# Performance work log

Hardware: AMD Instinct MI355X
Metric: run time of the kernel (lower is better)

## Reference

```python
import jax, jax.numpy as jnp
import numpy as np

V, E, H = 32000, 512, 1024
B, T = 32, 64

def setup_inputs() -> dict:
    key = jax.random.key(0)
    ks = jax.random.split(key, 8)
    return {
        "x": jax.random.randint(ks[0], (B, T), 0, V, dtype=jnp.int32),
        "state_h": jax.random.normal(ks[1], (B, H), dtype=jnp.float32),
        "state_c": jax.random.normal(ks[2], (B, H), dtype=jnp.float32),
        "emb_table": jax.random.normal(ks[3], (V, E), dtype=jnp.float32) * 0.02,
        "W": jax.random.normal(ks[4], (E, 4 * H), dtype=jnp.float32) * (1.0 / np.sqrt(E)),
        "U": jax.random.normal(ks[5], (H, 4 * H), dtype=jnp.float32) * (1.0 / np.sqrt(H)),
        "b": jnp.zeros((4 * H,), dtype=jnp.float32),
        "dense_W": jax.random.normal(ks[6], (H, V), dtype=jnp.float32) * (1.0 / np.sqrt(H)),
        "dense_b": jnp.zeros((V,), dtype=jnp.float32),
    }

def _lstm(emb, h0, c0, W, U, b):
    # Precompute input projections for all timesteps: [B,T,4H]
    xW = jnp.einsum('bte,eg->btg', emb, W) + b
    def step(carry, xw_t):
        h, c = carry
        z = xw_t + h @ U  # [B,4H]
        i, f, g, o = jnp.split(z, 4, axis=-1)  # Keras gate order i,f,c,o
        i = jax.nn.sigmoid(i)
        f = jax.nn.sigmoid(f)
        g = jnp.tanh(g)
        o = jax.nn.sigmoid(o)
        c = f * c + i * g
        h = o * jnp.tanh(c)
        return (h, c), h
    (h, c), hs = jax.lax.scan(step, (h0, c0), xW.transpose(1, 0, 2))
    return hs.transpose(1, 0, 2), h, c  # [B,T,H], [B,H], [B,H]

def reference(x, state_h, state_c, emb_table, W, U, b, dense_W, dense_b):
    emb = emb_table[x]  # [B,T,E]
    seq, h, c = _lstm(emb, state_h, state_c, W, U, b)
    logits = jnp.einsum('bth,hv->btv', seq, dense_W) + dense_b  # [B,T,V]
    return logits, h, c
```

## Files before the change

### kernel.cpp

```cpp
#include <hip/hip_runtime.h>

typedef unsigned short u16;
typedef __bf16 bf16x8 __attribute__((ext_vector_type(8)));
typedef float f32x4 __attribute__((ext_vector_type(4)));
typedef u16 u16x8 __attribute__((ext_vector_type(8)));
typedef u16 u16x4 __attribute__((ext_vector_type(4)));

#define T_STEPS 64
#define BATCH 32
#define HDIM 1024
#define EDIM 512
#define VDIM 32000
#define GDIM 4096

__device__ __forceinline__ u16 f2b(float v) {
  unsigned x = __float_as_uint(v);
  return (u16)((x + 0x7fffu + ((x >> 16) & 1u)) >> 16);
}

__device__ __forceinline__ void gload16(const void* g, void* l) {
  __builtin_amdgcn_global_load_lds(
      (const __attribute__((address_space(1))) void*)g,
      (__attribute__((address_space(3))) void*)l, 16, 0, 0);
}

__device__ __forceinline__ f32x4 mfma16(bf16x8 a, bf16x8 b, f32x4 c) {
  return __builtin_amdgcn_mfma_f32_16x16x32_bf16(a, b, c, 0, 0, 0);
}


__global__ __launch_bounds__(256) void gather_emb_k(
    const int* __restrict__ x, const float* __restrict__ emb,
    u16* __restrict__ A) {
  int bt = blockIdx.x;
  int tok = x[bt];
  const float4* src = (const float4*)(emb + (size_t)tok * EDIM);
  u16x4* dst = (u16x4*)(A + (size_t)bt * EDIM);
  if (threadIdx.x < 128) {
    float4 v = src[threadIdx.x];
    u16x4 o = {f2b(v.x), f2b(v.y), f2b(v.z), f2b(v.w)};
    dst[threadIdx.x] = o;
  }
}

__global__ __launch_bounds__(256) void transpose_cvt_k(
    const float* __restrict__ in, u16* __restrict__ out, int K, int N) {
  __shared__ float tile[64][65];
  int n0 = blockIdx.x * 64, k0 = blockIdx.y * 64;
  int tid = threadIdx.x;
  int r0 = tid >> 4;
  int c4 = (tid & 15) * 4;
#pragma unroll
  for (int rr = 0; rr < 4; ++rr) {
    int r = rr * 16 + r0;
    float4 v = *reinterpret_cast<const float4*>(
        &in[(size_t)(k0 + r) * N + n0 + c4]);
    *reinterpret_cast<float4*>(&tile[r][c4]) = v;
  }
  __syncthreads();
  int wr2 = tid >> 3, c8 = (tid & 7) * 8;
#pragma unroll
  for (int rr = 0; rr < 2; ++rr) {
    int r = rr * 32 + wr2;
    u16x8 o;
#pragma unroll
    for (int k = 0; k < 8; ++k) o[k] = f2b(tile[c8 + k][r]);
    *reinterpret_cast<u16x8*>(&out[(size_t)(n0 + r) * K + k0 + c8]) = o;
  }
}

__global__ __launch_bounds__(256) void transpose_cvt_permU_k(
    const float* __restrict__ in, u16* __restrict__ out) {
  const int K = HDIM, N = GDIM;
  __shared__ float tile[64][65];
  int n0 = blockIdx.x * 64, k0 = blockIdx.y * 64;
  int tid = threadIdx.x;
  int r0 = tid >> 4;
  int c4 = (tid & 15) * 4;
#pragma unroll
  for (int rr = 0; rr < 4; ++rr) {
    int r = rr * 16 + r0;
    float4 v = *reinterpret_cast<const float4*>(
        &in[(size_t)(k0 + r) * N + n0 + c4]);
    *reinterpret_cast<float4*>(&tile[r][c4]) = v;
  }
  __syncthreads();
  int wr2 = tid >> 3, c8 = (tid & 7) * 8;
#pragma unroll
  for (int rr = 0; rr < 2; ++rr) {
    int r = rr * 32 + wr2;
    int n = n0 + r;
    int g = n >> 10, c = n & 1023;
    int pn = ((c >> 2) << 4) + (g << 2) + (c & 3);
    u16x8 o;
#pragma unroll
    for (int k = 0; k < 8; ++k) o[k] = f2b(tile[c8 + k][r]);
    *reinterpret_cast<u16x8*>(&out[(size_t)pn * K + k0 + c8]) = o;
  }
}

__global__ __launch_bounds__(256) void init_state_k(
    const float* __restrict__ h0, const float* __restrict__ c0,
    u16* __restrict__ h0b, float* __restrict__ c_ws) {
  int i = blockIdx.x * 256 + threadIdx.x;
  h0b[i] = f2b(h0[i]);
  c_ws[i] = c0[i];
}


#define STG_A(dst, h, kb)                                              \
  do {                                                                 \
    gload16(Abytes + offA[h][0] + (kb), (dst) + (h) * 16384 + w * 1024); \
    gload16(Abytes + offA[h][1] + (kb),                                \
            (dst) + (h) * 16384 + 8192 + w * 1024);                    \
  } while (0)
#define STG_B(dst, h, kb)                                              \
  do {                                                                 \
    gload16(Bbytes + offB[h][0] + (kb),                                \
            (dst) + 32768 + (h) * 16384 + w * 1024);                   \
    gload16(Bbytes + offB[h][1] + (kb),                                \
            (dst) + 32768 + (h) * 16384 + 8192 + w * 1024);            \
  } while (0)
#define VMW4 asm volatile("s_waitcnt vmcnt(4)" ::: "memory")
#define VMW0 asm volatile("s_waitcnt vmcnt(0)" ::: "memory")

#define MFMA_BLOCK(mih)                                                   \
  do {                                                                    \
    __builtin_amdgcn_s_setprio(1);                                        \
    _Pragma("unroll") for (int u = 0; u < 4; ++u)                         \
        _Pragma("unroll") for (int v = 0; v < 4; ++v) {                   \
      acc[(mih)*4 + u][v] = mfma16(af[u][0], bfr[v][0], acc[(mih)*4 + u][v]); \
      acc[(mih)*4 + u][v] = mfma16(af[u][1], bfr[v][1], acc[(mih)*4 + u][v]); \
    }                                                                     \
    __builtin_amdgcn_s_setprio(0);                                        \
  } while (0)

#define PH_FULL(cur, mih, STG, WAIT)                                      \
  do {                                                                    \
    bf16x8 af[4][2];                                                      \
    _Pragma("unroll") for (int u = 0; u < 4; ++u) {                       \
      af[u][0] = *reinterpret_cast<const bf16x8*>((cur) +                 \
                                                  aoff[(mih)*4 + u][0]);  \
      af[u][1] = *reinterpret_cast<const bf16x8*>((cur) +                 \
                                                  aoff[(mih)*4 + u][1]);  \
    }                                                                     \
    _Pragma("unroll") for (int v = 0; v < 4; ++v) {                       \
      bfr[v][0] = *reinterpret_cast<const bf16x8*>((cur) + boff[v][0]);   \
      bfr[v][1] = *reinterpret_cast<const bf16x8*>((cur) + boff[v][1]);   \
    }                                                                     \
    STG;                                                                  \
    __builtin_amdgcn_s_barrier();                                         \
    asm volatile("s_waitcnt lgkmcnt(0)" ::: "memory");                    \
    MFMA_BLOCK(mih);                                                      \
    WAIT;                                                                 \
    __builtin_amdgcn_s_barrier();                                         \
  } while (0)

#define PH_A(cur, mih, STG, WAIT)                                         \
  do {                                                                    \
    bf16x8 af[4][2];                                                      \
    _Pragma("unroll") for (int u = 0; u < 4; ++u) {                       \
      af[u][0] = *reinterpret_cast<const bf16x8*>((cur) +                 \
                                                  aoff[(mih)*4 + u][0]);  \
      af[u][1] = *reinterpret_cast<const bf16x8*>((cur) +                 \
                                                  aoff[(mih)*4 + u][1]);  \
    }                                                                     \
    STG;                                                                  \
    __builtin_amdgcn_s_barrier();                                         \
    asm volatile("s_waitcnt lgkmcnt(0)" ::: "memory");                    \
    MFMA_BLOCK(mih);                                                      \
    WAIT;                                                                 \
    __builtin_amdgcn_s_barrier();                                         \
  } while (0)

__global__ __launch_bounds__(512, 2) void gemm256_k(
    const u16* __restrict__ A,
    const u16* __restrict__ BT,
    const float* __restrict__ bias,
    float* __restrict__ C,
    int M, int N, int K) {
  __shared__ __attribute__((aligned(1024))) char smem[131072];
  const int tid = threadIdx.x;
  const int w = tid >> 6, lane = tid & 63;
  const int lo16 = lane & 15, hi4 = lane >> 4;
  const int wr = w >> 2, wc = w & 3;

  const int cpx = gridDim.x >> 3;
  const int bid = blockIdx.x;
  const int swz = (bid & 7) * cpx + (bid >> 3);
  const int nmb = M >> 8;
  const int m0 = (swz % nmb) << 8, n0 = (swz / nmb) << 8;

  const char* Abytes = (const char*)A;
  const char* Bbytes = (const char*)BT;
  const int K2 = K * 2;

  int offA[2][2], offB[2][2];
#pragma unroll
  for (int h = 0; h < 2; ++h)
#pragma unroll
    for (int i = 0; i < 2; ++i) {
      int o = h * 16384 + (i * 512 + tid) * 16;
      int s = o >> 10, q = o & 1023;
      int qp = q ^ (((q >> 9) & 1) << 5);
      int row = ((s >> 1) << 4) + (qp >> 6);
      int colb = ((s & 1) << 6) + (qp & 63);
      offA[h][i] = (m0 + row) * K2 + colb;
      offB[h][i] = (n0 + row) * K2 + colb;
    }

  int aoff[8][2], boff[4][2];
#pragma unroll
  for (int mi = 0; mi < 8; ++mi)
#pragma unroll
    for (int kk = 0; kk < 2; ++kk) {
      int r = (mi >> 2) * 128 + wr * 64 + (mi & 3) * 16 + lo16;
      int q = (r & 15) * 64 + hi4 * 16;
      int qs = q ^ (((q >> 9) & 1) << 5);
      aoff[mi][kk] = (((r >> 4) << 1) + kk) * 1024 + qs;
    }
#pragma unroll
  for (int nj = 0; nj < 4; ++nj)
#pragma unroll
    for (int kk = 0; kk < 2; ++kk) {
      int r = (nj >> 1) * 128 + wc * 32 + (nj & 1) * 16 + lo16;
      int q = (r & 15) * 64 + hi4 * 16;
      int qs = q ^ (((q >> 9) & 1) << 5);
      boff[nj][kk] = 32768 + (((r >> 4) << 1) + kk) * 1024 + qs;
    }

  f32x4 acc[8][4] = {};
  bf16x8 bfr[4][2];
  char* const bd = smem;
  char* const bo = smem + 65536;

  STG_A(bd, 0, 0);
  STG_B(bd, 0, 0);
  STG_A(bd, 1, 0);
  STG_B(bd, 1, 0);
  STG_A(bo, 0, 128);
  STG_B(bo, 0, 128);
  VMW4;
  __builtin_amdgcn_s_barrier();

  const int NITER = K >> 7;
  for (int it = 0; it < NITER - 1; ++it) {
    const int k1 = (it * 128 + 64) * 2;
    const int k2 = (it * 128 + 128) * 2;
    const int k3 = (it * 128 + 192) * 2;
    PH_FULL(bd, 0, { STG_A(bo, 1, k1); STG_B(bo, 1, k1); }, ((void)0));
    PH_A(bd, 1, { STG_A(bd, 0, k2); STG_B(bd, 0, k2); }, VMW4);
    PH_FULL(bo, 0, { STG_A(bd, 1, k2); STG_B(bd, 1, k2); }, ((void)0));
    PH_A(bo, 1, { STG_A(bo, 0, k3); STG_B(bo, 0, k3); }, VMW4);
  }
  {
    const int k1 = ((NITER - 1) * 128 + 64) * 2;
    PH_FULL(bd, 0, { STG_A(bo, 1, k1); STG_B(bo, 1, k1); }, ((void)0));
    PH_A(bd, 1, ((void)0), VMW0);
    PH_FULL(bo, 0, ((void)0), ((void)0));
    PH_A(bo, 1, ((void)0), ((void)0));
  }

#pragma unroll
  for (int mi = 0; mi < 8; ++mi) {
    int row = m0 + (mi >> 2) * 128 + wr * 64 + (mi & 3) * 16 + hi4 * 4;
#pragma unroll
    for (int nj = 0; nj < 4; ++nj) {
      int col = n0 + (nj >> 1) * 128 + wc * 32 + (nj & 1) * 16 + lo16;
      float bv = bias ? bias[col] : 0.f;
#pragma unroll
      for (int j = 0; j < 4; ++j)
        C[(size_t)(row + j) * N + col] = acc[mi][nj][j] + bv;
    }
  }
}


__global__ __launch_bounds__(256) void lstm_step2_k(
    const float* __restrict__ xW,
    const u16* __restrict__ h_src,
    int h_stride,
    const u16* __restrict__ UT2,
    float* __restrict__ c_ws,
    u16* __restrict__ seq,
    float* __restrict__ out_hc,
    int t) {
  __shared__ float Zs[4][16][17];
  const int tid = threadIdx.x;
  const int w = tid >> 6, lane = tid & 63;
  const int lo16 = lane & 15, hi4 = lane >> 4;
  const int zt = blockIdx.x >> 1;
  const int bt = blockIdx.x & 1;

  const int bb = tid >> 2, jg = tid & 3;
  float xw0 = 0.f, xw1 = 0.f, xw2 = 0.f, xw3 = 0.f;
  if (tid < 64) {
    const float* xrow =
        xW + (size_t)((bt * 16 + bb) * T_STEPS + t) * GDIM + zt * 4 + jg;
    xw0 = xrow[0];
    xw1 = xrow[1024];
    xw2 = xrow[2048];
    xw3 = xrow[3072];
  }

  const u16* arow = h_src + (size_t)(bt * 16 + lo16) * h_stride;
  const u16* brow = UT2 + (size_t)(zt * 16 + lo16) * HDIM;

  f32x4 acc = {};
#pragma unroll
  for (int kc = 0; kc < 8; ++kc) {
    int k = w * 256 + kc * 32 + hi4 * 8;
    bf16x8 a = *reinterpret_cast<const bf16x8*>(arow + k);
    bf16x8 b = *reinterpret_cast<const bf16x8*>(brow + k);
    acc = mfma16(a, b, acc);
  }
#pragma unroll
  for (int j = 0; j < 4; ++j) Zs[w][hi4 * 4 + j][lo16] = acc[j];
  __syncthreads();

  if (tid < 64) {
    int b = bt * 16 + bb;
    int hcol = zt * 4 + jg;
    float z[4] = {xw0, xw1, xw2, xw3};
#pragma unroll
    for (int g = 0; g < 4; ++g)
#pragma unroll
      for (int ww = 0; ww < 4; ++ww) z[g] += Zs[ww][bb][g * 4 + jg];
    size_t cidx = (size_t)b * HDIM + hcol;
    float c_old = c_ws[cidx];
    float ig = 1.f / (1.f + __expf(-z[0]));
    float fg = 1.f / (1.f + __expf(-z[1]));
    float gg = tanhf(z[2]);
    float og = 1.f / (1.f + __expf(-z[3]));
    float cn = fg * c_old + ig * gg;
    float hn = og * tanhf(cn);
    c_ws[cidx] = cn;
    seq[(size_t)(b * T_STEPS + t) * HDIM + hcol] = f2b(hn);
    if (out_hc) {
      out_hc[cidx] = hn;
      out_hc[BATCH * HDIM + cidx] = cn;
    }
  }
}


extern "C" void kernel_launch(void* const* d_in, const int* in_sizes, int n_in,
                              void* d_out, int out_size, void* d_ws,
                              size_t ws_size, hipStream_t stream) {
  const int* x = (const int*)d_in[0];
  const float* state_h = (const float*)d_in[1];
  const float* state_c = (const float*)d_in[2];
  const float* emb = (const float*)d_in[3];
  const float* W = (const float*)d_in[4];
  const float* U = (const float*)d_in[5];
  const float* bvec = (const float*)d_in[6];
  const float* dW = (const float*)d_in[7];
  const float* db = (const float*)d_in[8];
  float* out = (float*)d_out;
  char* ws = (char*)d_ws;

  size_t off = 0;
  auto alloc = [&](size_t bytes) {
    void* p = ws + off;
    off += (bytes + 255) & ~(size_t)255;
    return p;
  };
  u16* A_emb = (u16*)alloc(2048ull * EDIM * 2);
  u16* WbT   = (u16*)alloc((size_t)GDIM * EDIM * 2);
  u16* UT2   = (u16*)alloc((size_t)GDIM * HDIM * 2);
  u16* DbT   = (u16*)alloc((size_t)VDIM * HDIM * 2);
  float* xW  = (float*)alloc(2048ull * GDIM * 4);
  u16* seq   = (u16*)alloc(2048ull * HDIM * 2);
  u16* h0b   = (u16*)alloc((size_t)BATCH * HDIM * 2);
  float* c_ws = (float*)alloc((size_t)BATCH * HDIM * 4);
  if (off > ws_size) return;

  gather_emb_k<<<2048, 256, 0, stream>>>(x, emb, A_emb);
  transpose_cvt_k<<<dim3(GDIM / 64, EDIM / 64), 256, 0, stream>>>(W, WbT, EDIM, GDIM);
  transpose_cvt_permU_k<<<dim3(GDIM / 64, HDIM / 64), 256, 0, stream>>>(U, UT2);
  transpose_cvt_k<<<dim3(VDIM / 64, HDIM / 64), 256, 0, stream>>>(dW, DbT, HDIM, VDIM);
  init_state_k<<<128, 256, 0, stream>>>(state_h, state_c, h0b, c_ws);

  gemm256_k<<<dim3((2048 / 256) * (GDIM / 256)), 512, 0, stream>>>(
      A_emb, WbT, bvec, xW, 2048, GDIM, EDIM);

  for (int t = 0; t < T_STEPS; ++t) {
    const u16* h_src = (t == 0) ? h0b : (seq + (size_t)(t - 1) * HDIM);
    int h_stride = (t == 0) ? HDIM : T_STEPS * HDIM;
    float* outhc = (t == T_STEPS - 1) ? (out + 65536000ull) : nullptr;
    lstm_step2_k<<<512, 256, 0, stream>>>(xW, h_src, h_stride, UT2, c_ws, seq,
                                          outhc, t);
  }

  gemm256_k<<<dim3((2048 / 256) * (VDIM / 256)), 512, 0, stream>>>(
      seq, DbT, db, out, 2048, VDIM, HDIM);
}
```

Measured before the change: 654.6 us.

## Stage GEMM epilogue through LDS, fuse gather/init kernels, use fast tanh

The GEMM epilogue now writes each wave's 16x64 accumulator tile into LDS and reads it back as float4 rows, so global stores are wide and coalesced instead of scattered scalar writes. This matters most for the large logits output. The embedding gather and state init are merged into one launch with two rows per block, and the LSTM cell uses an exp-based tanh instead of tanhf. Costs are extra LDS traffic and waits in the epilogue, plus slightly different tanh accuracy. The LDS reuse also relies on the main loop having finished with shared memory without an explicit block barrier.

```diff
diff --git a/kernel.cpp b/kernel.cpp
--- a/kernel.cpp
+++ b/kernel.cpp
@@ -18,6 +18,13 @@
   return (u16)((x + 0x7fffu + ((x >> 16) & 1u)) >> 16);
 }
 
+__device__ __forceinline__ float ftanh(float x) {
+  float ax = fabsf(x);
+  float e = __expf(2.f * ax);
+  float t = 1.f - 2.f / (e + 1.f);
+  return copysignf(t, x);
+}
+
 __device__ __forceinline__ void gload16(const void* g, void* l) {
   __builtin_amdgcn_global_load_lds(
       (const __attribute__((address_space(1))) void*)g,
@@ -29,17 +36,25 @@
 }
 
 
-__global__ __launch_bounds__(256) void gather_emb_k(
+__global__ __launch_bounds__(256) void gather_init_k(
     const int* __restrict__ x, const float* __restrict__ emb,
-    u16* __restrict__ A) {
-  int bt = blockIdx.x;
-  int tok = x[bt];
-  const float4* src = (const float4*)(emb + (size_t)tok * EDIM);
-  u16x4* dst = (u16x4*)(A + (size_t)bt * EDIM);
-  if (threadIdx.x < 128) {
-    float4 v = src[threadIdx.x];
+    u16* __restrict__ A, const float* __restrict__ h0,
+    const float* __restrict__ c0, u16* __restrict__ h0b,
+    float* __restrict__ c_ws) {
+  int tid = threadIdx.x;
+  if (blockIdx.x < 1024) {
+    int bt = blockIdx.x * 2 + (tid >> 7);
+    int tok = x[bt];
+    const float4* src = (const float4*)(emb + (size_t)tok * EDIM);
+    u16x4* dst = (u16x4*)(A + (size_t)bt * EDIM);
+    int i = tid & 127;
+    float4 v = src[i];
     u16x4 o = {f2b(v.x), f2b(v.y), f2b(v.z), f2b(v.w)};
-    dst[threadIdx.x] = o;
+    dst[i] = o;
+  } else {
+    int i = (blockIdx.x - 1024) * 256 + tid;
+    h0b[i] = f2b(h0[i]);
+    c_ws[i] = c0[i];
   }
 }
 
@@ -97,14 +112,6 @@
     for (int k = 0; k < 8; ++k) o[k] = f2b(tile[c8 + k][r]);
     *reinterpret_cast<u16x8*>(&out[(size_t)pn * K + k0 + c8]) = o;
   }
-}
-
-__global__ __launch_bounds__(256) void init_state_k(
-    const float* __restrict__ h0, const float* __restrict__ c0,
-    u16* __restrict__ h0b, float* __restrict__ c_ws) {
-  int i = blockIdx.x * 256 + threadIdx.x;
-  h0b[i] = f2b(h0[i]);
-  c_ws[i] = c0[i];
 }
 
 
@@ -261,17 +268,31 @@
     PH_A(bo, 1, ((void)0), ((void)0));
   }
 
+  float* lds_ep = reinterpret_cast<float*>(smem) + w * (16 * 66);
+  const int erow = lane >> 4;
+  const int ecol = lane & 15;
+  const int gcol = n0 + wc * 32 + ((ecol >= 8) ? 96 : 0) + ecol * 4;
 #pragma unroll
   for (int mi = 0; mi < 8; ++mi) {
-    int row = m0 + (mi >> 2) * 128 + wr * 64 + (mi & 3) * 16 + hi4 * 4;
+    int rowbase = m0 + (mi >> 2) * 128 + wr * 64 + (mi & 3) * 16;
 #pragma unroll
     for (int nj = 0; nj < 4; ++nj) {
-      int col = n0 + (nj >> 1) * 128 + wc * 32 + (nj & 1) * 16 + lo16;
-      float bv = bias ? bias[col] : 0.f;
+      int lc = (nj >> 1) * 32 + (nj & 1) * 16 + lo16;
+      float bv =
+          bias ? bias[n0 + (nj >> 1) * 128 + wc * 32 + (nj & 1) * 16 + lo16]
+               : 0.f;
 #pragma unroll
       for (int j = 0; j < 4; ++j)
-        C[(size_t)(row + j) * N + col] = acc[mi][nj][j] + bv;
-    }
+        lds_ep[(hi4 * 4 + j) * 66 + lc] = acc[mi][nj][j] + bv;
+    }
+    asm volatile("s_waitcnt lgkmcnt(0)" ::: "memory");
+#pragma unroll
+    for (int rr = 0; rr < 4; ++rr) {
+      int r = rr * 4 + erow;
+      float4 v = *reinterpret_cast<const float4*>(&lds_ep[r * 66 + ecol * 4]);
+      *reinterpret_cast<float4*>(&C[(size_t)(rowbase + r) * N + gcol]) = v;
+    }
+    asm volatile("s_waitcnt lgkmcnt(0)" ::: "memory");
   }
 }
 
@@ -330,10 +351,10 @@
     float c_old = c_ws[cidx];
     float ig = 1.f / (1.f + __expf(-z[0]));
     float fg = 1.f / (1.f + __expf(-z[1]));
-    float gg = tanhf(z[2]);
+    float gg = ftanh(z[2]);
     float og = 1.f / (1.f + __expf(-z[3]));
     float cn = fg * c_old + ig * gg;
-    float hn = og * tanhf(cn);
+    float hn = og * ftanh(cn);
     c_ws[cidx] = cn;
     seq[(size_t)(b * T_STEPS + t) * HDIM + hcol] = f2b(hn);
     if (out_hc) {
@@ -375,11 +396,11 @@
   float* c_ws = (float*)alloc((size_t)BATCH * HDIM * 4);
   if (off > ws_size) return;
 
-  gather_emb_k<<<2048, 256, 0, stream>>>(x, emb, A_emb);
+  gather_init_k<<<1152, 256, 0, stream>>>(x, emb, A_emb, state_h, state_c,
+                                          h0b, c_ws);
   transpose_cvt_k<<<dim3(GDIM / 64, EDIM / 64), 256, 0, stream>>>(W, WbT, EDIM, GDIM);
   transpose_cvt_permU_k<<<dim3(GDIM / 64, HDIM / 64), 256, 0, stream>>>(U, UT2);
   transpose_cvt_k<<<dim3(VDIM / 64, HDIM / 64), 256, 0, stream>>>(dW, DbT, HDIM, VDIM);
-  init_state_k<<<128, 256, 0, stream>>>(state_h, state_c, h0b, c_ws);
 
   gemm256_k<<<dim3((2048 / 256) * (GDIM / 256)), 512, 0, stream>>>(
       A_emb, WbT, bvec, xW, 2048, GDIM, EDIM);
```

Result: no change. 658.1 us (+0.5%).
